# Optimization experiments

Measured on AMD Instinct MI355X. Metric: run time of the kernel, lower is better.

The kernel has to match this reference:

```python
import jax, jax.numpy as jnp
import numpy as np

B, N, C, H = 8, 1024, 768, 12
D = C // H  # head_dim = 64
SCALE = D ** -0.5


def setup_inputs() -> dict:
    key = jax.random.key(0)
    ks = jax.random.split(key, 5)
    s = lambda k, sh, fan: jax.random.normal(k, sh, jnp.float32) * (fan ** -0.5)
    return {
        "x": jax.random.normal(ks[0], (B, N, C), jnp.float32),
        "w_qkv": s(ks[1], (C, 3 * C), C),
        "b_qkv": jnp.zeros((3 * C,), jnp.float32),
        "w_l": s(ks[2], (H, H), H),
        "b_l": jnp.zeros((H,), jnp.float32),
        "w_w": s(ks[3], (H, H), H),
        "b_w": jnp.zeros((H,), jnp.float32),
        "w_proj": s(ks[4], (C, C), C),
        "b_proj": jnp.zeros((C,), jnp.float32),
    }


def reference(x, w_qkv, b_qkv, w_l, b_l, w_w, b_w, w_proj, b_proj):
    Bq, Nq, Cq = x.shape
    # qkv projection -> (3, B, H, N, D)
    qkv = (x @ w_qkv + b_qkv).reshape(Bq, Nq, 3, H, D).transpose(2, 0, 3, 1, 4)
    q, k, v = qkv[0] * SCALE, qkv[1], qkv[2]
    # raw scores [B, H, N, N]
    attn = jnp.einsum("bhnd,bhmd->bhnm", q, k)
    # pre-softmax talking-heads: mix across head axis (Dense over H)
    attn = jnp.einsum("bhnm,hg->bgnm", attn, w_l) + b_l[None, :, None, None]
    attn = jax.nn.softmax(attn, axis=-1)
    # post-softmax talking-heads
    attn = jnp.einsum("bhnm,hg->bgnm", attn, w_w) + b_w[None, :, None, None]
    # weighted values -> (B, N, C)
    out = jnp.einsum("bhnm,bhmd->bnhd", attn, v).reshape(Bq, Nq, Cq)
    return out @ w_proj + b_proj
```

## Files before the change

kernel.cpp:

```cpp
#include <hip/hip_runtime.h>

#define BB 8
#define NN 1024
#define CC 768
#define HH 12
#define DD 64

typedef unsigned short u16;
typedef unsigned int u32;
typedef __attribute__((ext_vector_type(8))) short s16x8;
typedef __attribute__((ext_vector_type(4))) short s16x4;
typedef __attribute__((ext_vector_type(4))) float f32x4;
typedef __attribute__((ext_vector_type(2))) u32 u32x2;
typedef __attribute__((ext_vector_type(4))) u32 u32x4;

__device__ __forceinline__ float bf2f(u16 u) {
  u32 x = ((u32)u) << 16;
  return __builtin_bit_cast(float, x);
}
__device__ __forceinline__ u16 f2bf(float f) {
  u32 x = __builtin_bit_cast(u32, f);
  x += 0x7fffu + ((x >> 16) & 1u);
  return (u16)(x >> 16);
}
__device__ __forceinline__ float hw_exp2(float x) { return __builtin_amdgcn_exp2f(x); }
__device__ __forceinline__ float hw_log2(float x) { return __builtin_amdgcn_logf(x); }
__device__ __forceinline__ s16x8 lds_read8(const u16* p) {
  u32x2 a = *(const u32x2*)p;
  u32x2 b = *(const u32x2*)(p + 4);
  u32x4 m = {a.x, a.y, b.x, b.y};
  return __builtin_bit_cast(s16x8, m);
}
__device__ __forceinline__ u32 packhl(float v) {
  u32 xv = __builtin_bit_cast(u32, v);
  float lo = v - __builtin_bit_cast(float, xv & 0xFFFF0000u);
  return (xv >> 16) | (__builtin_bit_cast(u32, lo) & 0xFFFF0000u);
}
__device__ __forceinline__ void gload_lds16(const u16* g, u16* l) {
  __builtin_amdgcn_global_load_lds(
      (const __attribute__((address_space(1))) u32*)g,
      (__attribute__((address_space(3))) u32*)l, 16, 0, 0);
}

__global__ __launch_bounds__(256) void convx_kernel(const float* __restrict__ in,
                                                    u16* __restrict__ out) {
  size_t i = ((size_t)blockIdx.x * 256 + threadIdx.x) * 8;
  f32x4 a = *(const f32x4*)(in + i);
  f32x4 b = *(const f32x4*)(in + i + 4);
  s16x8 r;
#pragma unroll
  for (int j = 0; j < 4; j++) { r[j] = (short)f2bf(a[j]); r[4 + j] = (short)f2bf(b[j]); }
  *(s16x8*)(out + i) = r;
}

__global__ __launch_bounds__(256) void transpose_kernel(const float* __restrict__ in,
                                                        u16* __restrict__ out,
                                                        int R, int C) {
  __shared__ float t[32][33];
  const int cl = threadIdx.x & 31, rq = threadIdx.x >> 5;
#pragma unroll
  for (int rr = 0; rr < 4; rr++) {
    int rl = rq * 4 + rr;
    t[rl][cl] = in[(size_t)(blockIdx.y * 32 + rl) * C + blockIdx.x * 32 + cl];
  }
  __syncthreads();
#pragma unroll
  for (int rr = 0; rr < 4; rr++) {
    int oc = rq * 4 + rr;
    out[(size_t)(blockIdx.x * 32 + oc) * R + blockIdx.y * 32 + cl] = f2bf(t[cl][oc]);
  }
}

__global__ __launch_bounds__(256) void qkv_gemm(
    const u16* __restrict__ A, const u16* __restrict__ Bt, const float* __restrict__ bias,
    u16* __restrict__ qo, u16* __restrict__ ko, u16* __restrict__ vo) {
  __shared__ __align__(16) u16 As[2][128 * 32];
  __shared__ __align__(16) u16 Bs[2][128 * 32];
  const int tid = threadIdx.x;
  const int w = tid >> 6, lane = tid & 63, l15 = lane & 15, l4 = lane >> 4;
  const int wm = w & 1, wn = w >> 1;
  const int m0 = blockIdx.x * 128, n0 = blockIdx.y * 128;
  const int grow = lane >> 2, gcol = (lane & 3) * 8;

  const u16* ga0 = A + (size_t)(m0 + w * 32 + grow) * CC + gcol;
  const u16* gb0 = Bt + (size_t)(n0 + w * 32 + grow) * CC + gcol;

  f32x4 acc[4][4];
#pragma unroll
  for (int a = 0; a < 4; a++)
#pragma unroll
    for (int bb = 0; bb < 4; bb++) acc[a][bb] = (f32x4){0.f, 0.f, 0.f, 0.f};

  gload_lds16(ga0, &As[0][w * 1024]);
  gload_lds16(ga0 + (size_t)16 * CC, &As[0][w * 1024 + 512]);
  gload_lds16(gb0, &Bs[0][w * 1024]);
  gload_lds16(gb0 + (size_t)16 * CC, &Bs[0][w * 1024 + 512]);

  for (int t = 0; t < 24; ++t) {
    const int cb = t & 1, nb = cb ^ 1;
    if (t + 1 < 24) {
      const u16* ga = ga0 + (t + 1) * 32;
      const u16* gb = gb0 + (t + 1) * 32;
      gload_lds16(ga, &As[nb][w * 1024]);
      gload_lds16(ga + (size_t)16 * CC, &As[nb][w * 1024 + 512]);
      gload_lds16(gb, &Bs[nb][w * 1024]);
      gload_lds16(gb + (size_t)16 * CC, &Bs[nb][w * 1024 + 512]);
      asm volatile("s_waitcnt vmcnt(4)" ::: "memory");
    } else {
      asm volatile("s_waitcnt vmcnt(0)" ::: "memory");
    }
    __builtin_amdgcn_s_barrier();
    s16x8 af[4], bf[4];
#pragma unroll
    for (int a = 0; a < 4; a++) af[a] = *(const s16x8*)&As[cb][(wm * 64 + a * 16 + l15) * 32 + l4 * 8];
#pragma unroll
    for (int bb = 0; bb < 4; bb++) bf[bb] = *(const s16x8*)&Bs[cb][(wn * 64 + bb * 16 + l15) * 32 + l4 * 8];
#pragma unroll
    for (int a = 0; a < 4; a++)
#pragma unroll
      for (int bb = 0; bb < 4; bb++)
        acc[a][bb] = __builtin_amdgcn_mfma_f32_16x16x32_bf16(af[a], bf[bb], acc[a][bb], 0, 0, 0);
    asm volatile("s_waitcnt lgkmcnt(0)" ::: "memory");
    __builtin_amdgcn_s_barrier();
  }

  const int b = (m0 >> 10);
#pragma unroll
  for (int bb = 0; bb < 4; bb++) {
    int col = n0 + wn * 64 + bb * 16 + l15;
    int s = col / CC;
    int rem = col - s * CC;
    int h = rem >> 6, d = rem & 63;
    float bv = bias[col];
#pragma unroll
    for (int a = 0; a < 4; a++) {
      int row0 = m0 + wm * 64 + a * 16 + l4 * 4;
      int nt0 = row0 & (NN - 1);
      if (s == 2) {
        s16x4 pk;
#pragma unroll
        for (int r = 0; r < 4; r++) pk[r] = (short)f2bf(acc[a][bb][r] + bv);
        *(s16x4*)(vo + (((size_t)((b * HH + h) * DD + d)) << 10) + nt0) = pk;
      } else if (s == 0) {
#pragma unroll
        for (int r = 0; r < 4; r++)
          qo[(((size_t)((b * HH + h) * NN + nt0 + r)) << 6) + d] = f2bf((acc[a][bb][r] + bv) * 0.125f);
      } else {
#pragma unroll
        for (int r = 0; r < 4; r++)
          ko[(((size_t)((b * HH + h) * NN + nt0 + r)) << 6) + d] = f2bf(acc[a][bb][r] + bv);
      }
    }
  }
}

__global__ __launch_bounds__(256) void proj_gemm(
    const u16* __restrict__ A, const u16* __restrict__ Bt, const float* __restrict__ bias,
    float* __restrict__ out) {
  __shared__ __align__(16) u16 As[2][128 * 32];
  __shared__ __align__(16) u16 Bs[2][128 * 32];
  const int tid = threadIdx.x;
  const int w = tid >> 6, lane = tid & 63, l15 = lane & 15, l4 = lane >> 4;
  const int wm = w & 1, wn = w >> 1;
  const int m0 = blockIdx.x * 128, n0 = blockIdx.y * 128;
  const int grow = lane >> 2, gcol = (lane & 3) * 8;

  const u16* ga0 = A + (size_t)(m0 + w * 32 + grow) * CC + gcol;
  const u16* gb0 = Bt + (size_t)(n0 + w * 32 + grow) * CC + gcol;

  f32x4 acc[4][4];
#pragma unroll
  for (int a = 0; a < 4; a++)
#pragma unroll
    for (int bb = 0; bb < 4; bb++) acc[a][bb] = (f32x4){0.f, 0.f, 0.f, 0.f};

  gload_lds16(ga0, &As[0][w * 1024]);
  gload_lds16(ga0 + (size_t)16 * CC, &As[0][w * 1024 + 512]);
  gload_lds16(gb0, &Bs[0][w * 1024]);
  gload_lds16(gb0 + (size_t)16 * CC, &Bs[0][w * 1024 + 512]);

  for (int t = 0; t < 24; ++t) {
    const int cb = t & 1, nb = cb ^ 1;
    if (t + 1 < 24) {
      const u16* ga = ga0 + (t + 1) * 32;
      const u16* gb = gb0 + (t + 1) * 32;
      gload_lds16(ga, &As[nb][w * 1024]);
      gload_lds16(ga + (size_t)16 * CC, &As[nb][w * 1024 + 512]);
      gload_lds16(gb, &Bs[nb][w * 1024]);
      gload_lds16(gb + (size_t)16 * CC, &Bs[nb][w * 1024 + 512]);
      asm volatile("s_waitcnt vmcnt(4)" ::: "memory");
    } else {
      asm volatile("s_waitcnt vmcnt(0)" ::: "memory");
    }
    __builtin_amdgcn_s_barrier();
    s16x8 af[4], bf[4];
#pragma unroll
    for (int a = 0; a < 4; a++) af[a] = *(const s16x8*)&As[cb][(wm * 64 + a * 16 + l15) * 32 + l4 * 8];
#pragma unroll
    for (int bb = 0; bb < 4; bb++) bf[bb] = *(const s16x8*)&Bs[cb][(wn * 64 + bb * 16 + l15) * 32 + l4 * 8];
#pragma unroll
    for (int a = 0; a < 4; a++)
#pragma unroll
      for (int bb = 0; bb < 4; bb++)
        acc[a][bb] = __builtin_amdgcn_mfma_f32_16x16x32_bf16(af[a], bf[bb], acc[a][bb], 0, 0, 0);
    asm volatile("s_waitcnt lgkmcnt(0)" ::: "memory");
    __builtin_amdgcn_s_barrier();
  }

#pragma unroll
  for (int bb = 0; bb < 4; bb++) {
    int col = n0 + wn * 64 + bb * 16 + l15;
    float bv = bias[col];
#pragma unroll
    for (int a = 0; a < 4; a++) {
      int row0 = m0 + wm * 64 + a * 16 + l4 * 4;
#pragma unroll
      for (int r = 0; r < 4; r++)
        out[(size_t)(row0 + r) * CC + col] = acc[a][bb][r] + bv;
    }
  }
}

#define SB_BYTES 28736
#define UT_OFF   SB_BYTES
#define UT_ELE   6912
#define LL2_OFF  (SB_BYTES + 27648)
#define SM_TOTAL (LL2_OFF + 1088)

__global__ __launch_bounds__(512, 4) void attn_kernel(
    const u16* __restrict__ qg, const u16* __restrict__ kg, const u16* __restrict__ vtg,
    const float* __restrict__ wlg, const float* __restrict__ blg,
    const float* __restrict__ wwg, const float* __restrict__ bwg,
    u16* __restrict__ aout) {
  __shared__ __align__(16) char smem[SM_TOTAL];
  u16* Sb = (u16*)smem;
  u16* Ut0 = (u16*)(smem + UT_OFF);
  float* lpart = (float*)(smem + UT_OFF);
  float* ll2 = (float*)(smem + LL2_OFF);

  const int b = blockIdx.x, i0 = blockIdx.y * 16;
  const int tid = threadIdx.x;
  const int w = tid >> 6, lane = tid & 63, l15 = lane & 15, l4 = lane >> 4;
  const float RLN2 = 1.44269504088896340736f;

  for (int j = tid; j < SB_BYTES / 4; j += 512) ((u32*)smem)[j] = 0;
  __syncthreads();

  s16x8 wlS, wlA1, wlA2, wwA1, wwA2;
#pragma unroll
  for (int j = 0; j < 8; j++) {
    int k = l4 * 8 + j;
    float v1 = (k < 12 && l15 < 12) ? wlg[k * 12 + l15] * RLN2 : 0.f;
    wlS[j] = (short)f2bf(v1);
    int h = k >> 1, pt = k & 1;
    float v2 = (h < 12 && l15 < 12) ? wlg[h * 12 + l15] * RLN2 : 0.f;
    u16 h2 = f2bf(v2); u16 lo2 = f2bf(v2 - bf2f(h2));
    wlA1[j] = (short)h2; wlA2[j] = (short)(pt ? 0 : lo2);
    float v3 = (h < 12 && l15 < 12) ? wwg[h * 12 + l15] : 0.f;
    u16 h3 = f2bf(v3); u16 lo3 = f2bf(v3 - bf2f(h3));
    wwA1[j] = (short)h3; wwA2[j] = (short)(pt ? 0 : lo3);
  }
  int gr[4]; float blv[4], bwv[4];
#pragma unroll
  for (int r = 0; r < 4; r++) {
    gr[r] = l4 * 4 + r;
    blv[r] = (gr[r] < 12) ? blg[gr[r]] * RLN2 : 0.f;
    bwv[r] = (gr[r] < 12) ? bwg[gr[r]] : 0.f;
  }

  int jh[3], jmb[3];
  s16x8 qf[3][2];
#pragma unroll
  for (int jt = 0; jt < 3; jt++) {
    int j = w * 3 + jt;
    jh[jt] = j % 12; jmb[jt] = j / 12;
    const u16* qp = qg + (((size_t)((b * HH + jh[jt]) * NN + i0 + l15)) << 6) + l4 * 8;
    qf[jt][0] = *(const s16x8*)qp;
    qf[jt][1] = *(const s16x8*)(qp + 32);
  }

  float la[4] = {0.f, 0.f, 0.f, 0.f};
  for (int mt = 0; mt < 32; mt++) {
    const int m0 = mt * 32;
#pragma unroll
    for (int jt = 0; jt < 3; jt++) {
      const u16* kp = kg + (((size_t)((b * HH + jh[jt]) * NN + m0 + jmb[jt] * 16 + l15)) << 6) + l4 * 8;
      f32x4 ca = (f32x4){0.f, 0.f, 0.f, 0.f};
      f32x4 cb = (f32x4){0.f, 0.f, 0.f, 0.f};
      ca = __builtin_amdgcn_mfma_f32_16x16x32_bf16(*(const s16x8*)kp, qf[jt][0], ca, 0, 0, 0);
      cb = __builtin_amdgcn_mfma_f32_16x16x32_bf16(*(const s16x8*)(kp + 32), qf[jt][1], cb, 0, 0, 0);
      f32x4 c = ca + cb;
      int cbse = (jmb[jt] * 16 + l4 * 4) * 16 + l15;
#pragma unroll
      for (int r = 0; r < 4; r++)
        Sb[(size_t)(cbse + r * 16) * 20 + jh[jt]] = f2bf(c[r]);
    }
    __syncthreads();
#pragma unroll
    for (int tt = 0; tt < 4; tt++) {
      int t = w * 4 + tt;
      s16x8 bS = lds_read8(Sb + (size_t)(t * 16 + l15) * 20 + l4 * 8);
      f32x4 T = (f32x4){blv[0], blv[1], blv[2], blv[3]};
      T = __builtin_amdgcn_mfma_f32_16x16x32_bf16(wlS, bS, T, 0, 0, 0);
#pragma unroll
      for (int r = 0; r < 4; r++) la[r] += hw_exp2(T[r]);
    }
    __syncthreads();
  }

#pragma unroll
  for (int r = 0; r < 4; r++) lpart[w * 256 + gr[r] * 16 + l15] = la[r];
  __syncthreads();
  if (tid < 256) {
    float s = 0.f;
#pragma unroll
    for (int w2 = 0; w2 < 8; w2++) s += lpart[w2 * 256 + tid];
    ll2[(tid >> 4) * 17 + (tid & 15)] = hw_log2(s);
  }
  __syncthreads();
  float Tinit[4];
#pragma unroll
  for (int r = 0; r < 4; r++) Tinit[r] = blv[r] - ll2[gr[r] * 17 + l15];

  const int db = w >> 1, pvh = (w & 1) * 6;
  f32x4 O[6];
#pragma unroll
  for (int jp = 0; jp < 6; jp++) O[jp] = (f32x4){0.f, 0.f, 0.f, 0.f};

  for (int mt = 0; mt < 32; mt++) {
    const int m0 = mt * 32;
    u16* Utb = Ut0 + (mt & 1) * UT_ELE;
#pragma unroll
    for (int jt = 0; jt < 3; jt++) {
      const u16* kp = kg + (((size_t)((b * HH + jh[jt]) * NN + m0 + jmb[jt] * 16 + l15)) << 6) + l4 * 8;
      f32x4 ca = (f32x4){0.f, 0.f, 0.f, 0.f};
      f32x4 cb = (f32x4){0.f, 0.f, 0.f, 0.f};
      ca = __builtin_amdgcn_mfma_f32_16x16x32_bf16(*(const s16x8*)kp, qf[jt][0], ca, 0, 0, 0);
      cb = __builtin_amdgcn_mfma_f32_16x16x32_bf16(*(const s16x8*)(kp + 32), qf[jt][1], cb, 0, 0, 0);
      f32x4 c = ca + cb;
      int cbse = (jmb[jt] * 16 + l4 * 4) * 16 + l15;
#pragma unroll
      for (int r = 0; r < 4; r++)
        *(u32*)(Sb + (size_t)(cbse + r * 16) * 28 + 2 * jh[jt]) = packhl(c[r]);
    }
    __syncthreads();
#pragma unroll
    for (int tt = 0; tt < 4; tt++) {
      int t = w * 4 + tt;
      s16x8 bS = lds_read8(Sb + (size_t)(t * 16 + l15) * 28 + l4 * 8);
      f32x4 Ta = (f32x4){Tinit[0], Tinit[1], Tinit[2], Tinit[3]};
      f32x4 Tb = (f32x4){0.f, 0.f, 0.f, 0.f};
      Ta = __builtin_amdgcn_mfma_f32_16x16x32_bf16(wlA1, bS, Ta, 0, 0, 0);
      Tb = __builtin_amdgcn_mfma_f32_16x16x32_bf16(wlA2, bS, Tb, 0, 0, 0);
      f32x4 T = Ta + Tb;
      u32x4 pk;
#pragma unroll
      for (int r = 0; r < 4; r++) pk[r] = packhl(hw_exp2(T[r]));
      s16x8 bP = __builtin_bit_cast(s16x8, pk);
      f32x4 Ua = (f32x4){bwv[0], bwv[1], bwv[2], bwv[3]};
      f32x4 Ub = (f32x4){0.f, 0.f, 0.f, 0.f};
      Ua = __builtin_amdgcn_mfma_f32_16x16x32_bf16(wwA1, bP, Ua, 0, 0, 0);
      Ub = __builtin_amdgcn_mfma_f32_16x16x32_bf16(wwA2, bP, Ub, 0, 0, 0);
      f32x4 U = Ua + Ub;
#pragma unroll
      for (int r = 0; r < 4; r++)
        if (gr[r] < 12) Utb[(size_t)(gr[r] * 16 + l15) * 36 + t] = f2bf(U[r]);
    }
    __syncthreads();
#pragma unroll
    for (int jp = 0; jp < 6; jp++) {
      const int h = pvh + jp;
      s16x8 aV = *(const s16x8*)(vtg + (((size_t)((b * HH + h) * DD + db * 16 + l15)) << 10) + m0 + l4 * 8);
      s16x8 bU = lds_read8(Utb + (size_t)(h * 16 + l15) * 36 + l4 * 8);
      O[jp] = __builtin_amdgcn_mfma_f32_16x16x32_bf16(aV, bU, O[jp], 0, 0, 0);
    }
  }

#pragma unroll
  for (int jp = 0; jp < 6; jp++) {
    const int h = pvh + jp;
    const int d0 = db * 16 + l4 * 4;
    s16x4 pk4;
#pragma unroll
    for (int r = 0; r < 4; r++) pk4[r] = (short)f2bf(O[jp][r]);
    *(s16x4*)(aout + ((size_t)(b * NN) + i0 + l15) * CC + h * DD + d0) = pk4;
  }
}

extern "C" void kernel_launch(void* const* d_in, const int* in_sizes, int n_in,
                              void* d_out, int out_size, void* d_ws, size_t ws_size,
                              hipStream_t stream) {
  const float* x      = (const float*)d_in[0];
  const float* w_qkv  = (const float*)d_in[1];
  const float* b_qkv  = (const float*)d_in[2];
  const float* w_l    = (const float*)d_in[3];
  const float* b_l    = (const float*)d_in[4];
  const float* w_w    = (const float*)d_in[5];
  const float* b_w    = (const float*)d_in[6];
  const float* w_proj = (const float*)d_in[7];
  const float* b_proj = (const float*)d_in[8];

  const size_t per = (size_t)BB * HH * NN * DD;
  u16* xb  = (u16*)d_ws;
  u16* wqt = xb + per;
  u16* wpt = wqt + (size_t)3 * CC * CC;
  u16* q   = wpt + (size_t)CC * CC;
  u16* k   = q + per;
  u16* vt  = k + per;
  u16* ao  = vt + per;

  convx_kernel<<<3072, 256, 0, stream>>>(x, xb);
  transpose_kernel<<<dim3(3 * CC / 32, CC / 32), 256, 0, stream>>>(w_qkv, wqt, CC, 3 * CC);
  transpose_kernel<<<dim3(CC / 32, CC / 32), 256, 0, stream>>>(w_proj, wpt, CC, CC);
  qkv_gemm<<<dim3(64, 18), 256, 0, stream>>>(xb, wqt, b_qkv, q, k, vt);
  attn_kernel<<<dim3(BB, NN / 16), 512, 0, stream>>>(q, k, vt, w_l, b_l, w_w, b_w, ao);
  proj_gemm<<<dim3(64, 6), 256, 0, stream>>>(ao, wpt, b_proj, (float*)d_out);
}
```

Before: 446.0 us.

## Split attention into separate normalizer pass with key-split grid and main pass

New measurement: 485.0 us. 8.8% more time.

```diff
diff --git a/kernel.cpp b/kernel.cpp
--- a/kernel.cpp
+++ b/kernel.cpp
@@ -221,51 +221,36 @@
   }
 }
 
-#define SB_BYTES 28736
-#define UT_OFF   SB_BYTES
-#define UT_ELE   6912
-#define LL2_OFF  (SB_BYTES + 27648)
-#define SM_TOTAL (LL2_OFF + 1088)
-
-__global__ __launch_bounds__(512, 4) void attn_kernel(
-    const u16* __restrict__ qg, const u16* __restrict__ kg, const u16* __restrict__ vtg,
+
+#define P1_SB   20544
+#define P1_LP   (P1_SB)
+__global__ __launch_bounds__(512, 6) void attn_pass1(
+    const u16* __restrict__ qg, const u16* __restrict__ kg,
     const float* __restrict__ wlg, const float* __restrict__ blg,
-    const float* __restrict__ wwg, const float* __restrict__ bwg,
-    u16* __restrict__ aout) {
-  __shared__ __align__(16) char smem[SM_TOTAL];
+    float* __restrict__ lout) {
+  __shared__ __align__(16) char smem[P1_SB + 8192];
   u16* Sb = (u16*)smem;
-  u16* Ut0 = (u16*)(smem + UT_OFF);
-  float* lpart = (float*)(smem + UT_OFF);
-  float* ll2 = (float*)(smem + LL2_OFF);
-
-  const int b = blockIdx.x, i0 = blockIdx.y * 16;
+  float* lpart = (float*)(smem + P1_LP);
+
+  const int b = blockIdx.x, i0 = blockIdx.y * 16, s = blockIdx.z;
   const int tid = threadIdx.x;
   const int w = tid >> 6, lane = tid & 63, l15 = lane & 15, l4 = lane >> 4;
   const float RLN2 = 1.44269504088896340736f;
 
-  for (int j = tid; j < SB_BYTES / 4; j += 512) ((u32*)smem)[j] = 0;
+  for (int j = tid; j < P1_SB / 4; j += 512) ((u32*)smem)[j] = 0;
   __syncthreads();
 
-  s16x8 wlS, wlA1, wlA2, wwA1, wwA2;
+  s16x8 wlS;
 #pragma unroll
   for (int j = 0; j < 8; j++) {
     int k = l4 * 8 + j;
-    float v1 = (k < 12 && l15 < 12) ? wlg[k * 12 + l15] * RLN2 : 0.f;
-    wlS[j] = (short)f2bf(v1);
-    int h = k >> 1, pt = k & 1;
-    float v2 = (h < 12 && l15 < 12) ? wlg[h * 12 + l15] * RLN2 : 0.f;
-    u16 h2 = f2bf(v2); u16 lo2 = f2bf(v2 - bf2f(h2));
-    wlA1[j] = (short)h2; wlA2[j] = (short)(pt ? 0 : lo2);
-    float v3 = (h < 12 && l15 < 12) ? wwg[h * 12 + l15] : 0.f;
-    u16 h3 = f2bf(v3); u16 lo3 = f2bf(v3 - bf2f(h3));
-    wwA1[j] = (short)h3; wwA2[j] = (short)(pt ? 0 : lo3);
-  }
-  int gr[4]; float blv[4], bwv[4];
+    wlS[j] = (short)((k < 12 && l15 < 12) ? f2bf(wlg[k * 12 + l15] * RLN2) : 0);
+  }
+  float blv[4];
 #pragma unroll
   for (int r = 0; r < 4; r++) {
-    gr[r] = l4 * 4 + r;
-    blv[r] = (gr[r] < 12) ? blg[gr[r]] * RLN2 : 0.f;
-    bwv[r] = (gr[r] < 12) ? bwg[gr[r]] : 0.f;
+    int g = l4 * 4 + r;
+    blv[r] = (g < 12) ? blg[g] * RLN2 : 0.f;
   }
 
   int jh[3], jmb[3];
@@ -280,8 +265,8 @@
   }
 
   float la[4] = {0.f, 0.f, 0.f, 0.f};
-  for (int mt = 0; mt < 32; mt++) {
-    const int m0 = mt * 32;
+  for (int mt = 0; mt < 16; mt++) {
+    const int m0 = s * 512 + mt * 32;
 #pragma unroll
     for (int jt = 0; jt < 3; jt++) {
       const u16* kp = kg + (((size_t)((b * HH + jh[jt]) * NN + m0 + jmb[jt] * 16 + l15)) << 6) + l4 * 8;
@@ -309,14 +294,77 @@
   }
 
 #pragma unroll
-  for (int r = 0; r < 4; r++) lpart[w * 256 + gr[r] * 16 + l15] = la[r];
+  for (int r = 0; r < 4; r++) lpart[w * 256 + (l4 * 4 + r) * 16 + l15] = la[r];
   __syncthreads();
   if (tid < 256) {
-    float s = 0.f;
-#pragma unroll
-    for (int w2 = 0; w2 < 8; w2++) s += lpart[w2 * 256 + tid];
-    ll2[(tid >> 4) * 17 + (tid & 15)] = hw_log2(s);
-  }
+    float sum = 0.f;
+#pragma unroll
+    for (int w2 = 0; w2 < 8; w2++) sum += lpart[w2 * 256 + tid];
+    lout[(((size_t)(b * 64 + blockIdx.y) * 2 + s) << 8) + tid] = sum;
+  }
+}
+
+#define SB_BYTES 28736
+#define UT_OFF   SB_BYTES
+#define UT_ELE   6912
+#define LL2_OFF  (SB_BYTES + 27648)
+#define SM_TOTAL (LL2_OFF + 1088)
+
+__global__ __launch_bounds__(512, 4) void attn_pass2(
+    const u16* __restrict__ qg, const u16* __restrict__ kg, const u16* __restrict__ vtg,
+    const float* __restrict__ wlg, const float* __restrict__ blg,
+    const float* __restrict__ wwg, const float* __restrict__ bwg,
+    const float* __restrict__ lin, u16* __restrict__ aout) {
+  __shared__ __align__(16) char smem[SM_TOTAL];
+  u16* Sb = (u16*)smem;
+  u16* Ut0 = (u16*)(smem + UT_OFF);
+  float* ll2 = (float*)(smem + LL2_OFF);
+
+  const int b = blockIdx.x, i0 = blockIdx.y * 16;
+  const int tid = threadIdx.x;
+  const int w = tid >> 6, lane = tid & 63, l15 = lane & 15, l4 = lane >> 4;
+  const float RLN2 = 1.44269504088896340736f;
+
+  for (int j = tid; j < SB_BYTES / 4; j += 512) ((u32*)smem)[j] = 0;
+
+  if (tid < 256) {
+    size_t base = ((size_t)(b * 64 + blockIdx.y) * 2) << 8;
+    float l0 = lin[base + tid];
+    float l1 = lin[base + 256 + tid];
+    ll2[(tid >> 4) * 17 + (tid & 15)] = hw_log2(l0 + l1);
+  }
+
+  s16x8 wlA1, wlA2, wwA1, wwA2;
+#pragma unroll
+  for (int j = 0; j < 8; j++) {
+    int k = l4 * 8 + j;
+    int h = k >> 1, pt = k & 1;
+    float v2 = (h < 12 && l15 < 12) ? wlg[h * 12 + l15] * RLN2 : 0.f;
+    u16 h2 = f2bf(v2); u16 lo2 = f2bf(v2 - bf2f(h2));
+    wlA1[j] = (short)h2; wlA2[j] = (short)(pt ? 0 : lo2);
+    float v3 = (h < 12 && l15 < 12) ? wwg[h * 12 + l15] : 0.f;
+    u16 h3 = f2bf(v3); u16 lo3 = f2bf(v3 - bf2f(h3));
+    wwA1[j] = (short)h3; wwA2[j] = (short)(pt ? 0 : lo3);
+  }
+  int gr[4]; float blv[4], bwv[4];
+#pragma unroll
+  for (int r = 0; r < 4; r++) {
+    gr[r] = l4 * 4 + r;
+    blv[r] = (gr[r] < 12) ? blg[gr[r]] * RLN2 : 0.f;
+    bwv[r] = (gr[r] < 12) ? bwg[gr[r]] : 0.f;
+  }
+
+  int jh[3], jmb[3];
+  s16x8 qf[3][2];
+#pragma unroll
+  for (int jt = 0; jt < 3; jt++) {
+    int j = w * 3 + jt;
+    jh[jt] = j % 12; jmb[jt] = j / 12;
+    const u16* qp = qg + (((size_t)((b * HH + jh[jt]) * NN + i0 + l15)) << 6) + l4 * 8;
+    qf[jt][0] = *(const s16x8*)qp;
+    qf[jt][1] = *(const s16x8*)(qp + 32);
+  }
+
   __syncthreads();
   float Tinit[4];
 #pragma unroll
@@ -408,11 +456,13 @@
   u16* k   = q + per;
   u16* vt  = k + per;
   u16* ao  = vt + per;
+  float* lw = (float*)(ao + per);
 
   convx_kernel<<<3072, 256, 0, stream>>>(x, xb);
   transpose_kernel<<<dim3(3 * CC / 32, CC / 32), 256, 0, stream>>>(w_qkv, wqt, CC, 3 * CC);
   transpose_kernel<<<dim3(CC / 32, CC / 32), 256, 0, stream>>>(w_proj, wpt, CC, CC);
   qkv_gemm<<<dim3(64, 18), 256, 0, stream>>>(xb, wqt, b_qkv, q, k, vt);
-  attn_kernel<<<dim3(BB, NN / 16), 512, 0, stream>>>(q, k, vt, w_l, b_l, w_w, b_w, ao);
+  attn_pass1<<<dim3(BB, NN / 16, 2), 512, 0, stream>>>(q, k, w_l, b_l, lw);
+  attn_pass2<<<dim3(BB, NN / 16), 512, 0, stream>>>(q, k, vt, w_l, b_l, w_w, b_w, lw, ao);
   proj_gemm<<<dim3(64, 6), 256, 0, stream>>>(ao, wpt, b_proj, (float*)d_out);
 }
```
